# Performance work log

Hardware: AMD Instinct MI355X
Metric: run time of the kernel (lower is better)

Reference implementation:

```python
import jax, jax.numpy as jnp
import numpy as np

NUM_HEADS = 16
HEAD_DIM = 64
MAX_MEM = 4 * 4096
TOP_K = 8
EPS = 1e-8


def _l2norm(x, eps=EPS):
    # matches torch F.normalize(p=2, dim=-1, eps): x / max(||x||, eps)
    n = jnp.sqrt(jnp.sum(x * x, axis=-1, keepdims=True))
    return x / jnp.maximum(n, eps)


def setup_inputs() -> dict:
    key0 = jax.random.key(0)
    ks = jax.random.split(key0, 8)
    B, S, D = 2, 512, 1024
    H, hd = NUM_HEADS, HEAD_DIM
    return {
        "inputs": jax.random.normal(ks[0], (B, S, D), dtype=jnp.float32),
        "query": jax.random.normal(ks[1], (B, H, S, hd), dtype=jnp.float32),
        "key": jax.random.normal(ks[2], (B, H, S, hd), dtype=jnp.float32),
        "value": jax.random.normal(ks[3], (B, H, S, hd), dtype=jnp.float32),
        "outputs": jax.random.normal(ks[4], (B, H, S, hd), dtype=jnp.float32),
        "gate": jnp.zeros((H,), dtype=jnp.float32),  # nn.Parameter init zeros
        "key_memories": jax.random.normal(ks[5], (H, MAX_MEM, hd), dtype=jnp.float32),
        "value_memories": jax.random.normal(ks[6], (H, MAX_MEM, hd), dtype=jnp.float32),
    }


def reference(inputs, query, key, value, outputs, gate, key_memories, value_memories):
    B, S, _ = inputs.shape
    H = query.shape[1]
    hd = HEAD_DIM

    # [B,H,S,d] -> [H, B*S, d]
    q = jnp.transpose(query, (1, 0, 2, 3)).reshape(H, B * S, hd)

    # --- KNN lookup (no_grad in original) ---
    qn = _l2norm(q)                    # [H, N, d]
    kn = _l2norm(key_memories)         # [H, M, d]
    sims = jnp.einsum("hnd,hmd->hnm", qn, kn) / jnp.sqrt(jnp.float32(hd))
    scores, indices = jax.lax.top_k(sims, TOP_K)  # [H, N, k]

    # gather memory values per head: [H, N, k, d]
    mem_vals = jax.vmap(lambda vm, ix: vm[ix])(value_memories, indices)

    # weighted sum over k neighbors
    weighted = jnp.sum(mem_vals * scores[..., None], axis=2)  # [H, N, d]
    weighted = weighted.reshape(H, B, S, hd).transpose(1, 0, 2, 3)  # [B,H,S,d]

    g = jax.nn.sigmoid(gate).reshape(1, H, 1, 1)
    out_dim = outputs.shape[-1]
    combined = g * weighted[..., :out_dim] + (1.0 - g) * outputs
    return combined
```

## Files before the change

kernel.cpp:

```cpp
#include <hip/hip_runtime.h>
#include <math.h>

#define NHEADS 16
#define HD 64
#define MMEM 16384
#define NQ 1024
#define SEQ 512
#define EPS 1e-8f
#define NPART 8
#define NT 64
#define CMAX 16

typedef short bf16x8 __attribute__((ext_vector_type(8)));
typedef float f32x16 __attribute__((ext_vector_type(16)));

__device__ inline unsigned short f2bf(float f) {
    unsigned int u = __builtin_bit_cast(unsigned int, f);
    unsigned int r = (u + 0x7FFFu + ((u >> 16) & 1u)) >> 16;
    return (unsigned short)r;
}

__device__ inline unsigned vkey(float v) {
    float f = fmaf(v, 0.125f, 2.0f);
    f = fminf(fmaxf(f, 1.0f), 3.9999998f);
    return (__builtin_bit_cast(unsigned, f) - 0x3F800000u) >> 8;
}
__device__ inline float vunkey(unsigned k) {
    float f = __builtin_bit_cast(float, (k << 8) + 0x3F800000u);
    return (f - 2.0f) * 8.0f;
}

#define SS(Q) (Q.x*Q.x + Q.y*Q.y + Q.z*Q.z + Q.w*Q.w)

__global__ __launch_bounds__(256)
void kprep_kernel(const float* __restrict__ kmem,
                  float* __restrict__ knr,
                  unsigned short* __restrict__ kbf) {
    __shared__ float ssl[256];
    const int tid = threadIdx.x;
    const int gid = blockIdx.x * 256 + tid;
    const int lane = gid & 63;
    const int ks   = (gid >> 6) & 3;
    const int t    = (gid >> 8) & 511;
    const int h    = gid >> 17;
    const int r    = lane & 31;
    const int hi   = lane >> 5;
    const int row  = t * 32 + r;
    const int d0   = ks * 16 + hi * 8;

    const float* src = kmem + (((size_t)h * MMEM + row) << 6) + d0;
    float4 v0 = *(const float4*)(src);
    float4 v1 = *(const float4*)(src + 4);
    float ss = SS(v0) + SS(v1);
    ssl[r * 8 + ks * 2 + hi] = ss;
    __syncthreads();
    float tot = ssl[r*8+0] + ssl[r*8+1] + ssl[r*8+2] + ssl[r*8+3]
              + ssl[r*8+4] + ssl[r*8+5] + ssl[r*8+6] + ssl[r*8+7];
    const float rn = 1.0f / fmaxf(sqrtf(tot), EPS);
    if (ks == 0 && hi == 0) knr[h * MMEM + row] = rn;

    uint4 o;
    o.x = (unsigned)f2bf(v0.x * rn) | ((unsigned)f2bf(v0.y * rn) << 16);
    o.y = (unsigned)f2bf(v0.z * rn) | ((unsigned)f2bf(v0.w * rn) << 16);
    o.z = (unsigned)f2bf(v1.x * rn) | ((unsigned)f2bf(v1.y * rn) << 16);
    o.w = (unsigned)f2bf(v1.z * rn) | ((unsigned)f2bf(v1.w * rn) << 16);
    *(uint4*)(kbf + (size_t)gid * 8) = o;
}

#define MAX16(ACC)                                                            \
    fmaxf(fmaxf(fmaxf(fmaxf(ACC[0],ACC[1]),fmaxf(ACC[2],ACC[3])),             \
                fmaxf(fmaxf(ACC[4],ACC[5]),fmaxf(ACC[6],ACC[7]))),            \
          fmaxf(fmaxf(fmaxf(ACC[8],ACC[9]),fmaxf(ACC[10],ACC[11])),           \
                fmaxf(fmaxf(ACC[12],ACC[13]),fmaxf(ACC[14],ACC[15]))))

__device__ inline void ins8(float (&tv)[8], float v) {
#pragma unroll
    for (int j = 0; j < 8; ++j) {
        float h_ = fmaxf(tv[j], v);
        float l_ = fminf(tv[j], v);
        tv[j] = h_;
        v = l_;
    }
}

__device__ inline void ins8u(unsigned (&tv)[8], unsigned v) {
#pragma unroll
    for (int j = 0; j < 8; ++j) {
        unsigned h_ = tv[j] > v ? tv[j] : v;
        unsigned l_ = tv[j] > v ? v : tv[j];
        tv[j] = h_;
        v = l_;
    }
}

__device__ inline void ins8u64(unsigned long long (&tv)[8], unsigned long long v) {
#pragma unroll
    for (int j = 0; j < 8; ++j) {
        unsigned long long h_ = tv[j] > v ? tv[j] : v;
        unsigned long long l_ = tv[j] > v ? v : tv[j];
        tv[j] = h_;
        v = l_;
    }
}

__device__ inline bf16x8 pack8f(float4 a, float4 b) {
    bf16x8 f;
    f[0] = (short)f2bf(a.x); f[1] = (short)f2bf(a.y);
    f[2] = (short)f2bf(a.z); f[3] = (short)f2bf(a.w);
    f[4] = (short)f2bf(b.x); f[5] = (short)f2bf(b.y);
    f[6] = (short)f2bf(b.z); f[7] = (short)f2bf(b.w);
    return f;
}

#define MFMA8(AF0, AF1, AF2, AF3)                                             \
    f32x16 accA = {0,0,0,0,0,0,0,0,0,0,0,0,0,0,0,0};                         \
    f32x16 accB = {0,0,0,0,0,0,0,0,0,0,0,0,0,0,0,0};                         \
    accA = __builtin_amdgcn_mfma_f32_32x32x16_bf16(AF0, qA[0], accA, 0, 0, 0);\
    accB = __builtin_amdgcn_mfma_f32_32x32x16_bf16(AF0, qB[0], accB, 0, 0, 0);\
    accA = __builtin_amdgcn_mfma_f32_32x32x16_bf16(AF1, qA[1], accA, 0, 0, 0);\
    accB = __builtin_amdgcn_mfma_f32_32x32x16_bf16(AF1, qB[1], accB, 0, 0, 0);\
    accA = __builtin_amdgcn_mfma_f32_32x32x16_bf16(AF2, qA[2], accA, 0, 0, 0);\
    accB = __builtin_amdgcn_mfma_f32_32x32x16_bf16(AF2, qB[2], accB, 0, 0, 0);\
    accA = __builtin_amdgcn_mfma_f32_32x32x16_bf16(AF3, qA[3], accA, 0, 0, 0);\
    accB = __builtin_amdgcn_mfma_f32_32x32x16_bf16(AF3, qB[3], accB, 0, 0, 0);

__global__ __launch_bounds__(64, 4)
void scanA_kernel(const float* __restrict__ query,
                  const unsigned short* __restrict__ kbf,
                  uint4* __restrict__ pkeys) {
    const int lane = threadIdx.x;
    int bid = blockIdx.x;
    const int p  = bid & 7;   bid >>= 3;
    const int qg = bid & 15;  bid >>= 4;
    const int h  = bid;
    const int col = lane & 31;
    const int hi  = lane >> 5;
    const int n0  = qg * 64 + col;
    const int n1  = n0 + 32;

    bf16x8 qA[4], qB[4];
    {
        const int b0 = n0 >> 9, s0 = n0 & 511;
        const int b1 = n1 >> 9, s1 = n1 & 511;
        const float* qp0 = query + ((((size_t)b0 * NHEADS + h) * SEQ + s0) << 6);
        const float* qp1 = query + ((((size_t)b1 * NHEADS + h) * SEQ + s1) << 6);
#pragma unroll
        for (int ks = 0; ks < 4; ++ks) {
            const int d0 = ks * 16 + hi * 8;
            qA[ks] = pack8f(*(const float4*)(qp0 + d0), *(const float4*)(qp0 + d0 + 4));
            qB[ks] = pack8f(*(const float4*)(qp1 + d0), *(const float4*)(qp1 + d0 + 4));
        }
    }

    float tvA[8], tvB[8];
#pragma unroll
    for (int j = 0; j < 8; ++j) { tvA[j] = -1e30f; tvB[j] = -1e30f; }

    const unsigned char* ptr = (const unsigned char*)kbf
        + ((size_t)h * 512 + (size_t)p * NT) * 4096 + (size_t)lane * 16;

    bf16x8 aX0, aX1, aX2, aX3, aY0, aY1, aY2, aY3;
    aX0 = *(const bf16x8*)(ptr);
    aX1 = *(const bf16x8*)(ptr + 1024);
    aX2 = *(const bf16x8*)(ptr + 2048);
    aX3 = *(const bf16x8*)(ptr + 3072);

#pragma unroll 1
    for (int t = 0; t < NT; t += 2) {
        {
            const unsigned char* pn = ptr + (size_t)(t + 1) * 4096;
            aY0 = *(const bf16x8*)(pn);
            aY1 = *(const bf16x8*)(pn + 1024);
            aY2 = *(const bf16x8*)(pn + 2048);
            aY3 = *(const bf16x8*)(pn + 3072);
        }
        {
            MFMA8(aX0, aX1, aX2, aX3)
            ins8(tvA, MAX16(accA));
            ins8(tvB, MAX16(accB));
        }
        if (t + 2 < NT) {
            const unsigned char* p2 = ptr + (size_t)(t + 2) * 4096;
            aX0 = *(const bf16x8*)(p2);
            aX1 = *(const bf16x8*)(p2 + 1024);
            aX2 = *(const bf16x8*)(p2 + 2048);
            aX3 = *(const bf16x8*)(p2 + 3072);
        }
        {
            MFMA8(aY0, aY1, aY2, aY3)
            ins8(tvA, MAX16(accA));
            ins8(tvB, MAX16(accB));
        }
    }

    const int g = p * 2 + hi;
    uint4 oA, oB;
    oA.x = vkey(tvA[0]) | (vkey(tvA[1]) << 16);
    oA.y = vkey(tvA[2]) | (vkey(tvA[3]) << 16);
    oA.z = vkey(tvA[4]) | (vkey(tvA[5]) << 16);
    oA.w = vkey(tvA[6]) | (vkey(tvA[7]) << 16);
    oB.x = vkey(tvB[0]) | (vkey(tvB[1]) << 16);
    oB.y = vkey(tvB[2]) | (vkey(tvB[3]) << 16);
    oB.z = vkey(tvB[4]) | (vkey(tvB[5]) << 16);
    oB.w = vkey(tvB[6]) | (vkey(tvB[7]) << 16);
    pkeys[((size_t)h * NQ + n0) * 16 + g] = oA;
    pkeys[((size_t)h * NQ + n1) * 16 + g] = oB;
}

__global__ __launch_bounds__(256)
void taured_kernel(const uint4* __restrict__ pkeys,
                   float* __restrict__ tauv) {
    const int gid = blockIdx.x * 256 + threadIdx.x;
    unsigned tvk[8];
#pragma unroll
    for (int j = 0; j < 8; ++j) tvk[j] = 0u;
#pragma unroll
    for (int k = 0; k < 16; ++k) {
        uint4 v = pkeys[(size_t)gid * 16 + k];
        ins8u(tvk, v.x & 0xFFFFu); ins8u(tvk, v.x >> 16);
        ins8u(tvk, v.y & 0xFFFFu); ins8u(tvk, v.y >> 16);
        ins8u(tvk, v.z & 0xFFFFu); ins8u(tvk, v.z >> 16);
        ins8u(tvk, v.w & 0xFFFFu); ins8u(tvk, v.w >> 16);
    }
    tauv[gid] = vunkey(tvk[7]);
}

__global__ __launch_bounds__(64, 4)
void scanB_kernel(const float* __restrict__ query,
                  const unsigned short* __restrict__ kbf,
                  const float* __restrict__ tauv,
                  unsigned* __restrict__ pcand,
                  unsigned* __restrict__ pcnt) {
    const int lane = threadIdx.x;
    int bid = blockIdx.x;
    const int p  = bid & 7;   bid >>= 3;
    const int qg = bid & 15;  bid >>= 4;
    const int h  = bid;
    const int col = lane & 31;
    const int hi  = lane >> 5;
    const int n0  = qg * 64 + col;
    const int n1  = n0 + 32;

    bf16x8 qA[4], qB[4];
    float ssA = 0.f, ssB = 0.f;
    {
        const int b0 = n0 >> 9, s0 = n0 & 511;
        const int b1 = n1 >> 9, s1 = n1 & 511;
        const float* qp0 = query + ((((size_t)b0 * NHEADS + h) * SEQ + s0) << 6);
        const float* qp1 = query + ((((size_t)b1 * NHEADS + h) * SEQ + s1) << 6);
#pragma unroll
        for (int ks = 0; ks < 4; ++ks) {
            const int d0 = ks * 16 + hi * 8;
            float4 a0 = *(const float4*)(qp0 + d0), b0v = *(const float4*)(qp0 + d0 + 4);
            float4 a1 = *(const float4*)(qp1 + d0), b1v = *(const float4*)(qp1 + d0 + 4);
            ssA += SS(a0) + SS(b0v);
            ssB += SS(a1) + SS(b1v);
            qA[ks] = pack8f(a0, b0v);
            qB[ks] = pack8f(a1, b1v);
        }
    }
    ssA += __shfl_xor(ssA, 32);
    ssB += __shfl_xor(ssB, 32);
    const float tA = tauv[h * NQ + n0] - (sqrtf(ssA) * 0.0078125f + 0.01f);
    const float tB = tauv[h * NQ + n1] - (sqrtf(ssB) * 0.0078125f + 0.01f);

    const unsigned char* ptr = (const unsigned char*)kbf
        + ((size_t)h * 512 + (size_t)p * NT) * 4096 + (size_t)lane * 16;

    unsigned cA = 0, cB = 0;
    const size_t chA = ((size_t)h * NQ + n0) * 16 + p * 2 + hi;
    const size_t chB = ((size_t)h * NQ + n1) * 16 + p * 2 + hi;
    unsigned* mApt = pcand + chA * CMAX;
    unsigned* mBpt = pcand + chB * CMAX;

#define EMITM(ACC, TAU, C, LST, MBV) do {                                     \
        unsigned _msk = 0;                                                    \
        _Pragma("unroll")                                                     \
        for (int _r = 0; _r < 16; ++_r)                                       \
            _msk |= (ACC[_r] >= (TAU)) ? (1u << _r) : 0u;                     \
        if (_msk) {                                                           \
            do {                                                              \
                int _r = __ffs(_msk) - 1;                                     \
                unsigned _idx = (unsigned)((MBV) + (_r & 3) + 8 * (_r >> 2)); \
                if ((C) < CMAX) (LST)[C] = _idx;                              \
                ++(C);                                                        \
                _msk &= _msk - 1;                                             \
            } while (_msk);                                                   \
        }                                                                     \
    } while (0)

    bf16x8 aX0, aX1, aX2, aX3, aY0, aY1, aY2, aY3;
    aX0 = *(const bf16x8*)(ptr);
    aX1 = *(const bf16x8*)(ptr + 1024);
    aX2 = *(const bf16x8*)(ptr + 2048);
    aX3 = *(const bf16x8*)(ptr + 3072);

#pragma unroll 1
    for (int t = 0; t < NT; t += 2) {
        {
            const unsigned char* pn = ptr + (size_t)(t + 1) * 4096;
            aY0 = *(const bf16x8*)(pn);
            aY1 = *(const bf16x8*)(pn + 1024);
            aY2 = *(const bf16x8*)(pn + 2048);
            aY3 = *(const bf16x8*)(pn + 3072);
        }
        {
            MFMA8(aX0, aX1, aX2, aX3)
            const int mbv = p * 2048 + t * 32 + 4 * hi;
            EMITM(accA, tA, cA, mApt, mbv);
            EMITM(accB, tB, cB, mBpt, mbv);
        }
        if (t + 2 < NT) {
            const unsigned char* p2 = ptr + (size_t)(t + 2) * 4096;
            aX0 = *(const bf16x8*)(p2);
            aX1 = *(const bf16x8*)(p2 + 1024);
            aX2 = *(const bf16x8*)(p2 + 2048);
            aX3 = *(const bf16x8*)(p2 + 3072);
        }
        {
            MFMA8(aY0, aY1, aY2, aY3)
            const int mbv = p * 2048 + (t + 1) * 32 + 4 * hi;
            EMITM(accA, tA, cA, mApt, mbv);
            EMITM(accB, tB, cB, mBpt, mbv);
        }
    }
    pcnt[chA] = cA;
    pcnt[chB] = cB;
#undef EMITM
}

__global__ __launch_bounds__(64, 8)
void rescore_merge_kernel(const float* __restrict__ query,
                          const float* __restrict__ kmem,
                          const float* __restrict__ knr,
                          const unsigned* __restrict__ pcand,
                          const unsigned* __restrict__ pcnt,
                          const float* __restrict__ vmem,
                          const float* __restrict__ outputs,
                          const float* __restrict__ gate,
                          float* __restrict__ out) {
    __shared__ unsigned cands[16 * CMAX];
    const int gid = blockIdx.x;
    const int h = gid >> 10;
    const int n = gid & 1023;
    const int b = n >> 9;
    const int s = n & 511;
    const int lane = threadIdx.x;
    const int d4 = lane & 15;

    const float* qbase = query + ((((size_t)b * NHEADS + h) * SEQ + s) << 6);
    const float4 q4 = ((const float4*)qbase)[d4];
    float ssp = SS(q4);
    ssp += __shfl_xor(ssp, 1);
    ssp += __shfl_xor(ssp, 2);
    ssp += __shfl_xor(ssp, 4);
    ssp += __shfl_xor(ssp, 8);
    const float qs = 1.0f / (fmaxf(sqrtf(ssp), EPS) * 8.0f);

    const unsigned cg = pcnt[(size_t)gid * 16 + d4];
    const bool anyovf = (__ballot(cg > CMAX) != 0ULL);
    unsigned inc = cg;
#pragma unroll
    for (int d = 1; d < 16; d <<= 1) {
        unsigned t = __shfl_up(inc, d, 16);
        if (d4 >= d) inc += t;
    }
    const unsigned ct = __shfl(inc, 15, 16);
    const unsigned excl = inc - cg;
    if (lane < 16) {
        const unsigned* lp = pcand + ((size_t)gid * 16 + lane) * CMAX;
        const unsigned cc = cg > CMAX ? CMAX : cg;
        for (unsigned c = 0; c < cc; ++c) cands[excl + c] = lp[c];
    }
    __syncthreads();

    const float* kb = kmem + ((size_t)h << 20);
    const float* nb = knr + h * MMEM;

    unsigned long long top[8];
#pragma unroll
    for (int j = 0; j < 8; ++j) top[j] = 0ULL;

#define SCORE_KEY(IDX) ({                                                     \
        float4 kv = ((const float4*)(kb + ((size_t)(IDX) << 6)))[d4];         \
        float d = q4.x*kv.x + q4.y*kv.y + q4.z*kv.z + q4.w*kv.w;              \
        d += __shfl_xor(d, 1);                                                \
        d += __shfl_xor(d, 2);                                                \
        d += __shfl_xor(d, 4);                                                \
        d += __shfl_xor(d, 8);                                                \
        const float sc = d * qs * nb[IDX];                                    \
        unsigned su = __builtin_bit_cast(unsigned, sc);                       \
        unsigned ms = su ^ ((su >> 31) ? 0xFFFFFFFFu : 0x80000000u);          \
        ((unsigned long long)ms << 32) | (0xFFFFFFFFu - (unsigned)(IDX));     \
    })

    if (!anyovf) {
#pragma unroll 1
        for (unsigned c = 0; c < ct; ++c) {
            const unsigned idx = cands[c];
            ins8u64(top, SCORE_KEY(idx));
        }
    } else {
#pragma unroll 1
        for (int m = 0; m < MMEM; ++m) ins8u64(top, SCORE_KEY(m));
    }
#undef SCORE_KEY

    float acc = 0.0f;
    const float* vb = vmem + ((size_t)h << 20);
#pragma unroll
    for (int j = 0; j < 8; ++j) {
        const unsigned long long key = top[j];
        const unsigned idx = 0xFFFFFFFFu - (unsigned)(key & 0xFFFFFFFFu);
        const unsigned ms = (unsigned)(key >> 32);
        const unsigned su = ms ^ ((ms >> 31) ? 0x80000000u : 0xFFFFFFFFu);
        const float sc = __builtin_bit_cast(float, su);
        acc = fmaf(sc, vb[((size_t)idx << 6) + lane], acc);
    }

    const float gg = 1.0f / (1.0f + expf(-gate[h]));
    const size_t off = ((((size_t)b * NHEADS + h) * SEQ + s) << 6) + lane;
    out[off] = gg * acc + (1.0f - gg) * outputs[off];
}

__global__ void knorm_kernel(const float* __restrict__ kmem,
                             float* __restrict__ knr) {
    int gid = blockIdx.x * 256 + threadIdx.x;
    int mem = gid >> 4;
    int d4  = gid & 15;
    float4 kv = reinterpret_cast<const float4*>(kmem)[(size_t)mem * 16 + d4];
    float ss = SS(kv);
    ss += __shfl_xor(ss, 1);
    ss += __shfl_xor(ss, 2);
    ss += __shfl_xor(ss, 4);
    ss += __shfl_xor(ss, 8);
    if (d4 == 0) knr[mem] = 1.0f / fmaxf(sqrtf(ss), EPS);
}

__global__ __launch_bounds__(64, 4)
void scan_kernel(const float* __restrict__ query,
                 const float* __restrict__ kmem,
                 const float* __restrict__ knr,
                 float* __restrict__ pscore,
                 int* __restrict__ pidx,
                 int P, int CH) {
    const int lane = threadIdx.x & 63;
    int bid = blockIdx.x;
    const int p  = bid % P;  bid /= P;
    const int qb = bid & 15; bid >>= 4;
    const int h  = bid;
    const int n  = qb * 64 + lane;
    const int b  = n >> 9;
    const int s  = n & 511;

    const float4* qp = reinterpret_cast<const float4*>(
        query + (((size_t)b * NHEADS + h) * SEQ + s) * HD);
    float q[HD];
    float ss = 0.0f;
#pragma unroll
    for (int i = 0; i < 16; ++i) {
        float4 v = qp[i];
        q[4*i+0] = v.x; q[4*i+1] = v.y; q[4*i+2] = v.z; q[4*i+3] = v.w;
        ss += SS(v);
    }
    const float rq = 1.0f / (fmaxf(sqrtf(ss), EPS) * 8.0f);
#pragma unroll
    for (int i = 0; i < HD; ++i) q[i] *= rq;

    float tv[8]; int ti[8];
#pragma unroll
    for (int j = 0; j < 8; ++j) { tv[j] = -INFINITY; ti[j] = 0; }

    const int m0 = p * CH;
    const float4* kp = reinterpret_cast<const float4*>(
        kmem + ((size_t)h * MMEM + m0) * HD);
    const float* knrp = knr + h * MMEM + m0;

    for (int mm = 0; mm < CH; ++mm) {
        float d0 = 0.f, d1 = 0.f, d2 = 0.f, d3 = 0.f;
#pragma unroll
        for (int i = 0; i < 16; ++i) {
            float4 kv = kp[(size_t)mm * 16 + i];
            d0 = fmaf(q[4*i+0], kv.x, d0);
            d1 = fmaf(q[4*i+1], kv.y, d1);
            d2 = fmaf(q[4*i+2], kv.z, d2);
            d3 = fmaf(q[4*i+3], kv.w, d3);
        }
        const float sim = ((d0 + d1) + (d2 + d3)) * knrp[mm];
        if (sim > tv[7]) {
            tv[7] = sim; ti[7] = m0 + mm;
#pragma unroll
            for (int j = 7; j > 0; --j) {
                if (tv[j] > tv[j-1]) {
                    float tf = tv[j]; tv[j] = tv[j-1]; tv[j-1] = tf;
                    int   tu = ti[j]; ti[j] = ti[j-1]; ti[j-1] = tu;
                }
            }
        }
    }

    const size_t base = (((size_t)h * NQ + n) * P + p) * 8;
#pragma unroll
    for (int j = 0; j < 8; ++j) { pscore[base+j] = tv[j]; pidx[base+j] = ti[j]; }
}

__global__ void merge_kernel(const float* __restrict__ pscore,
                             const int* __restrict__ pidx,
                             const float* __restrict__ vmem,
                             const float* __restrict__ outputs,
                             const float* __restrict__ gate,
                             float* __restrict__ out, int P) {
    const int t = blockIdx.x * 256 + threadIdx.x;
    const int h = t >> 10;
    const int n = t & 1023;
    const int b = n >> 9;
    const int s = n & 511;

    float tv[8]; int ti[8];
    const size_t base = ((size_t)h * NQ + n) * P * 8;
#pragma unroll
    for (int j = 0; j < 8; ++j) { tv[j] = pscore[base + j]; ti[j] = pidx[base + j]; }
    const int total = P * 8;
    for (int c = 8; c < total; ++c) {
        const float v = pscore[base + c];
        if (v > tv[7]) {
            tv[7] = v; ti[7] = pidx[base + c];
#pragma unroll
            for (int j = 7; j > 0; --j) {
                if (tv[j] > tv[j-1]) {
                    float tf = tv[j]; tv[j] = tv[j-1]; tv[j-1] = tf;
                    int   tu = ti[j]; ti[j] = ti[j-1]; ti[j-1] = tu;
                }
            }
        }
    }

    float4 acc[16];
#pragma unroll
    for (int i = 0; i < 16; ++i) acc[i] = make_float4(0.f, 0.f, 0.f, 0.f);
#pragma unroll
    for (int j = 0; j < 8; ++j) {
        const float4* vp = reinterpret_cast<const float4*>(
            vmem + ((size_t)h * MMEM + ti[j]) * HD);
        const float sc = tv[j];
#pragma unroll
        for (int i = 0; i < 16; ++i) {
            float4 v = vp[i];
            acc[i].x = fmaf(sc, v.x, acc[i].x);
            acc[i].y = fmaf(sc, v.y, acc[i].y);
            acc[i].z = fmaf(sc, v.z, acc[i].z);
            acc[i].w = fmaf(sc, v.w, acc[i].w);
        }
    }

    const float g  = 1.0f / (1.0f + expf(-gate[h]));
    const float og = 1.0f - g;
    const size_t off = (((size_t)b * NHEADS + h) * SEQ + s) * HD;
    const float4* op = reinterpret_cast<const float4*>(outputs + off);
    float4* dst = reinterpret_cast<float4*>(out + off);
#pragma unroll
    for (int i = 0; i < 16; ++i) {
        float4 o = op[i];
        float4 r;
        r.x = g * acc[i].x + og * o.x;
        r.y = g * acc[i].y + og * o.y;
        r.z = g * acc[i].z + og * o.z;
        r.w = g * acc[i].w + og * o.w;
        dst[i] = r;
    }
}

extern "C" void kernel_launch(void* const* d_in, const int* in_sizes, int n_in,
                              void* d_out, int out_size, void* d_ws, size_t ws_size,
                              hipStream_t stream) {
    const float* query   = (const float*)d_in[1];
    const float* outputs = (const float*)d_in[4];
    const float* gate    = (const float*)d_in[5];
    const float* kmem    = (const float*)d_in[6];
    const float* vmem    = (const float*)d_in[7];
    float* out = (float*)d_out;

    const size_t NQTOT    = (size_t)NHEADS * NQ;
    const size_t sz_knr   = (size_t)NHEADS * MMEM * 4;
    const size_t sz_kbf   = (size_t)NHEADS * MMEM * HD * 2;
    const size_t sz_pkeys = NQTOT * 16 * 16;
    const size_t sz_tauv  = NQTOT * 4;
    const size_t sz_pcand = NQTOT * 16 * CMAX * 4;
    const size_t sz_pcnt  = NQTOT * 16 * 4;
    const size_t need = sz_knr + sz_kbf + sz_pkeys + sz_tauv + sz_pcand + sz_pcnt;

    if (ws_size >= need) {
        char* w = (char*)d_ws;
        float*          knr   = (float*)w;          w += sz_knr;
        unsigned short* kbf   = (unsigned short*)w; w += sz_kbf;
        uint4*          pkeys = (uint4*)w;          w += sz_pkeys;
        float*          tauv  = (float*)w;          w += sz_tauv;
        unsigned*       pcand = (unsigned*)w;       w += sz_pcand;
        unsigned*       pcnt  = (unsigned*)w;

        kprep_kernel<<<(NHEADS * 512 * 4 * 64) / 256, 256, 0, stream>>>(kmem, knr, kbf);
        scanA_kernel<<<NHEADS * 16 * NPART, 64, 0, stream>>>(query, kbf, pkeys);
        taured_kernel<<<(int)(NQTOT / 256), 256, 0, stream>>>(pkeys, tauv);
        scanB_kernel<<<NHEADS * 16 * NPART, 64, 0, stream>>>(query, kbf, tauv, pcand, pcnt);
        rescore_merge_kernel<<<(int)NQTOT, 64, 0, stream>>>(
            query, kmem, knr, pcand, pcnt, vmem, outputs, gate, out);
    } else {
        int P = 16;
        while (P > 4 &&
               (size_t)NHEADS * MMEM * 4 + (size_t)NHEADS * NQ * (size_t)P * 64 > ws_size)
            P >>= 1;
        const int CH = MMEM / P;

        float* knr    = (float*)d_ws;
        float* pscore = knr + (size_t)NHEADS * MMEM;
        int*   pidx   = (int*)(pscore + (size_t)NHEADS * NQ * (size_t)P * 8);

        knorm_kernel<<<(NHEADS * MMEM * 16) / 256, 256, 0, stream>>>(kmem, knr);
        scan_kernel<<<NHEADS * 16 * P, 64, 0, stream>>>(
            query, kmem, knr, pscore, pidx, P, CH);
        merge_kernel<<<(NHEADS * NQ) / 256, 256, 0, stream>>>(
            pscore, pidx, vmem, outputs, gate, out, P);
    }
}
```

Measured before the change: 168.8 us.

## Use per-group maxima for top-k threshold and double scan partitions

Measured after the change: 149.7 us. -11.3%, faster.

```diff
diff --git a/kernel.cpp b/kernel.cpp
--- a/kernel.cpp
+++ b/kernel.cpp
@@ -7,9 +7,10 @@
 #define NQ 1024
 #define SEQ 512
 #define EPS 1e-8f
-#define NPART 8
-#define NT 64
-#define CMAX 16
+#define NPART 16
+#define NT 32
+#define NGRP 32
+#define CMAX 8
 
 typedef short bf16x8 __attribute__((ext_vector_type(8)));
 typedef float f32x16 __attribute__((ext_vector_type(16)));
@@ -18,16 +19,6 @@
     unsigned int u = __builtin_bit_cast(unsigned int, f);
     unsigned int r = (u + 0x7FFFu + ((u >> 16) & 1u)) >> 16;
     return (unsigned short)r;
-}
-
-__device__ inline unsigned vkey(float v) {
-    float f = fmaf(v, 0.125f, 2.0f);
-    f = fminf(fmaxf(f, 1.0f), 3.9999998f);
-    return (__builtin_bit_cast(unsigned, f) - 0x3F800000u) >> 8;
-}
-__device__ inline float vunkey(unsigned k) {
-    float f = __builtin_bit_cast(float, (k << 8) + 0x3F800000u);
-    return (f - 2.0f) * 8.0f;
 }
 
 #define SS(Q) (Q.x*Q.x + Q.y*Q.y + Q.z*Q.z + Q.w*Q.w)
@@ -52,10 +43,20 @@
     float4 v0 = *(const float4*)(src);
     float4 v1 = *(const float4*)(src + 4);
     float ss = SS(v0) + SS(v1);
-    ssl[r * 8 + ks * 2 + hi] = ss;
+    const int lr = tid >> 6;
+    ssl[lr * 64 + r * 2 + 0] = 0.f;
     __syncthreads();
-    float tot = ssl[r*8+0] + ssl[r*8+1] + ssl[r*8+2] + ssl[r*8+3]
-              + ssl[r*8+4] + ssl[r*8+5] + ssl[r*8+6] + ssl[r*8+7];
+    ssl[(tid & 192)  + r * 2 + (ks & 1) + 0] = 0.f;
+    __syncthreads();
+    ssl[(tid >> 6) * 64 + r * 2 + ((ks * 2 + hi) & 1)] = 0.f;
+    __syncthreads();
+    ssl[tid] = ss;
+    __syncthreads();
+    const int base = (tid & 192) | (r ? 0 : 0);
+    float tot = ssl[0 * 64 + r] + ssl[0 * 64 + 32 + r]
+              + ssl[1 * 64 + r] + ssl[1 * 64 + 32 + r]
+              + ssl[2 * 64 + r] + ssl[2 * 64 + 32 + r]
+              + ssl[3 * 64 + r] + ssl[3 * 64 + 32 + r];
     const float rn = 1.0f / fmaxf(sqrtf(tot), EPS);
     if (ks == 0 && hi == 0) knr[h * MMEM + row] = rn;
 
@@ -78,16 +79,6 @@
     for (int j = 0; j < 8; ++j) {
         float h_ = fmaxf(tv[j], v);
         float l_ = fminf(tv[j], v);
-        tv[j] = h_;
-        v = l_;
-    }
-}
-
-__device__ inline void ins8u(unsigned (&tv)[8], unsigned v) {
-#pragma unroll
-    for (int j = 0; j < 8; ++j) {
-        unsigned h_ = tv[j] > v ? tv[j] : v;
-        unsigned l_ = tv[j] > v ? v : tv[j];
         tv[j] = h_;
         v = l_;
     }
@@ -124,13 +115,28 @@
     accA = __builtin_amdgcn_mfma_f32_32x32x16_bf16(AF3, qA[3], accA, 0, 0, 0);\
     accB = __builtin_amdgcn_mfma_f32_32x32x16_bf16(AF3, qB[3], accB, 0, 0, 0);
 
+#define LOADQ()                                                               \
+    bf16x8 qA[4], qB[4];                                                      \
+    {                                                                         \
+        const int b0 = n0 >> 9, s0 = n0 & 511;                                \
+        const int b1 = n1 >> 9, s1 = n1 & 511;                                \
+        const float* qp0 = query + ((((size_t)b0 * NHEADS + h) * SEQ + s0) << 6); \
+        const float* qp1 = query + ((((size_t)b1 * NHEADS + h) * SEQ + s1) << 6); \
+        _Pragma("unroll")                                                     \
+        for (int ks = 0; ks < 4; ++ks) {                                      \
+            const int d0 = ks * 16 + hi * 8;                                  \
+            qA[ks] = pack8f(*(const float4*)(qp0 + d0), *(const float4*)(qp0 + d0 + 4)); \
+            qB[ks] = pack8f(*(const float4*)(qp1 + d0), *(const float4*)(qp1 + d0 + 4)); \
+        }                                                                     \
+    }
+
 __global__ __launch_bounds__(64, 4)
 void scanA_kernel(const float* __restrict__ query,
                   const unsigned short* __restrict__ kbf,
-                  uint4* __restrict__ pkeys) {
+                  float* __restrict__ pmax) {
     const int lane = threadIdx.x;
     int bid = blockIdx.x;
-    const int p  = bid & 7;   bid >>= 3;
+    const int p  = bid & 15;  bid >>= 4;
     const int qg = bid & 15;  bid >>= 4;
     const int h  = bid;
     const int col = lane & 31;
@@ -138,23 +144,9 @@
     const int n0  = qg * 64 + col;
     const int n1  = n0 + 32;
 
-    bf16x8 qA[4], qB[4];
-    {
-        const int b0 = n0 >> 9, s0 = n0 & 511;
-        const int b1 = n1 >> 9, s1 = n1 & 511;
-        const float* qp0 = query + ((((size_t)b0 * NHEADS + h) * SEQ + s0) << 6);
-        const float* qp1 = query + ((((size_t)b1 * NHEADS + h) * SEQ + s1) << 6);
-#pragma unroll
-        for (int ks = 0; ks < 4; ++ks) {
-            const int d0 = ks * 16 + hi * 8;
-            qA[ks] = pack8f(*(const float4*)(qp0 + d0), *(const float4*)(qp0 + d0 + 4));
-            qB[ks] = pack8f(*(const float4*)(qp1 + d0), *(const float4*)(qp1 + d0 + 4));
-        }
-    }
-
-    float tvA[8], tvB[8];
-#pragma unroll
-    for (int j = 0; j < 8; ++j) { tvA[j] = -1e30f; tvB[j] = -1e30f; }
+    LOADQ()
+
+    float gA = -1e30f, gB = -1e30f;
 
     const unsigned char* ptr = (const unsigned char*)kbf
         + ((size_t)h * 512 + (size_t)p * NT) * 4096 + (size_t)lane * 16;
@@ -176,8 +168,8 @@
         }
         {
             MFMA8(aX0, aX1, aX2, aX3)
-            ins8(tvA, MAX16(accA));
-            ins8(tvB, MAX16(accB));
+            gA = fmaxf(gA, MAX16(accA));
+            gB = fmaxf(gB, MAX16(accB));
         }
         if (t + 2 < NT) {
             const unsigned char* p2 = ptr + (size_t)(t + 2) * 4096;
@@ -188,41 +180,26 @@
         }
         {
             MFMA8(aY0, aY1, aY2, aY3)
-            ins8(tvA, MAX16(accA));
-            ins8(tvB, MAX16(accB));
+            gA = fmaxf(gA, MAX16(accA));
+            gB = fmaxf(gB, MAX16(accB));
         }
     }
 
     const int g = p * 2 + hi;
-    uint4 oA, oB;
-    oA.x = vkey(tvA[0]) | (vkey(tvA[1]) << 16);
-    oA.y = vkey(tvA[2]) | (vkey(tvA[3]) << 16);
-    oA.z = vkey(tvA[4]) | (vkey(tvA[5]) << 16);
-    oA.w = vkey(tvA[6]) | (vkey(tvA[7]) << 16);
-    oB.x = vkey(tvB[0]) | (vkey(tvB[1]) << 16);
-    oB.y = vkey(tvB[2]) | (vkey(tvB[3]) << 16);
-    oB.z = vkey(tvB[4]) | (vkey(tvB[5]) << 16);
-    oB.w = vkey(tvB[6]) | (vkey(tvB[7]) << 16);
-    pkeys[((size_t)h * NQ + n0) * 16 + g] = oA;
-    pkeys[((size_t)h * NQ + n1) * 16 + g] = oB;
+    pmax[(((size_t)h * NQ + n0) << 5) + g] = gA;
+    pmax[(((size_t)h * NQ + n1) << 5) + g] = gB;
 }
 
 __global__ __launch_bounds__(256)
-void taured_kernel(const uint4* __restrict__ pkeys,
+void taured_kernel(const float* __restrict__ pmax,
                    float* __restrict__ tauv) {
     const int gid = blockIdx.x * 256 + threadIdx.x;
-    unsigned tvk[8];
-#pragma unroll
-    for (int j = 0; j < 8; ++j) tvk[j] = 0u;
-#pragma unroll
-    for (int k = 0; k < 16; ++k) {
-        uint4 v = pkeys[(size_t)gid * 16 + k];
-        ins8u(tvk, v.x & 0xFFFFu); ins8u(tvk, v.x >> 16);
-        ins8u(tvk, v.y & 0xFFFFu); ins8u(tvk, v.y >> 16);
-        ins8u(tvk, v.z & 0xFFFFu); ins8u(tvk, v.z >> 16);
-        ins8u(tvk, v.w & 0xFFFFu); ins8u(tvk, v.w >> 16);
-    }
-    tauv[gid] = vunkey(tvk[7]);
+    float tv[8];
+#pragma unroll
+    for (int j = 0; j < 8; ++j) tv[j] = -1e30f;
+#pragma unroll
+    for (int k = 0; k < NGRP; ++k) ins8(tv, pmax[((size_t)gid << 5) + k]);
+    tauv[gid] = tv[7];
 }
 
 __global__ __launch_bounds__(64, 4)
@@ -233,7 +210,7 @@
                   unsigned* __restrict__ pcnt) {
     const int lane = threadIdx.x;
     int bid = blockIdx.x;
-    const int p  = bid & 7;   bid >>= 3;
+    const int p  = bid & 15;  bid >>= 4;
     const int qg = bid & 15;  bid >>= 4;
     const int h  = bid;
     const int col = lane & 31;
@@ -268,8 +245,8 @@
         + ((size_t)h * 512 + (size_t)p * NT) * 4096 + (size_t)lane * 16;
 
     unsigned cA = 0, cB = 0;
-    const size_t chA = ((size_t)h * NQ + n0) * 16 + p * 2 + hi;
-    const size_t chB = ((size_t)h * NQ + n1) * 16 + p * 2 + hi;
+    const size_t chA = (((size_t)h * NQ + n0) << 5) + p * 2 + hi;
+    const size_t chB = (((size_t)h * NQ + n1) << 5) + p * 2 + hi;
     unsigned* mApt = pcand + chA * CMAX;
     unsigned* mBpt = pcand + chB * CMAX;
 
@@ -306,7 +283,7 @@
         }
         {
             MFMA8(aX0, aX1, aX2, aX3)
-            const int mbv = p * 2048 + t * 32 + 4 * hi;
+            const int mbv = p * 1024 + t * 32 + 4 * hi;
             EMITM(accA, tA, cA, mApt, mbv);
             EMITM(accB, tB, cB, mBpt, mbv);
         }
@@ -319,7 +296,7 @@
         }
         {
             MFMA8(aY0, aY1, aY2, aY3)
-            const int mbv = p * 2048 + (t + 1) * 32 + 4 * hi;
+            const int mbv = p * 1024 + (t + 1) * 32 + 4 * hi;
             EMITM(accA, tA, cA, mApt, mbv);
             EMITM(accB, tB, cB, mBpt, mbv);
         }
@@ -339,7 +316,7 @@
                           const float* __restrict__ outputs,
                           const float* __restrict__ gate,
                           float* __restrict__ out) {
-    __shared__ unsigned cands[16 * CMAX];
+    __shared__ unsigned cands[NGRP * CMAX];
     const int gid = blockIdx.x;
     const int h = gid >> 10;
     const int n = gid & 1023;
@@ -347,6 +324,7 @@
     const int s = n & 511;
     const int lane = threadIdx.x;
     const int d4 = lane & 15;
+    const int d5 = lane & 31;
 
     const float* qbase = query + ((((size_t)b * NHEADS + h) * SEQ + s) << 6);
     const float4 q4 = ((const float4*)qbase)[d4];
@@ -357,18 +335,18 @@
     ssp += __shfl_xor(ssp, 8);
     const float qs = 1.0f / (fmaxf(sqrtf(ssp), EPS) * 8.0f);
 
-    const unsigned cg = pcnt[(size_t)gid * 16 + d4];
+    const unsigned cg = pcnt[((size_t)gid << 5) + d5];
     const bool anyovf = (__ballot(cg > CMAX) != 0ULL);
     unsigned inc = cg;
 #pragma unroll
-    for (int d = 1; d < 16; d <<= 1) {
-        unsigned t = __shfl_up(inc, d, 16);
-        if (d4 >= d) inc += t;
-    }
-    const unsigned ct = __shfl(inc, 15, 16);
+    for (int d = 1; d < 32; d <<= 1) {
+        unsigned t = __shfl_up(inc, d, 32);
+        if (d5 >= d) inc += t;
+    }
+    const unsigned ct = __shfl(inc, 31, 32);
     const unsigned excl = inc - cg;
-    if (lane < 16) {
-        const unsigned* lp = pcand + ((size_t)gid * 16 + lane) * CMAX;
+    if (lane < 32) {
+        const unsigned* lp = pcand + (((size_t)gid << 5) + lane) * CMAX;
         const unsigned cc = cg > CMAX ? CMAX : cg;
         for (unsigned c = 0; c < cc; ++c) cands[excl + c] = lp[c];
     }
@@ -583,24 +561,24 @@
     const size_t NQTOT    = (size_t)NHEADS * NQ;
     const size_t sz_knr   = (size_t)NHEADS * MMEM * 4;
     const size_t sz_kbf   = (size_t)NHEADS * MMEM * HD * 2;
-    const size_t sz_pkeys = NQTOT * 16 * 16;
+    const size_t sz_pmax  = NQTOT * NGRP * 4;
     const size_t sz_tauv  = NQTOT * 4;
-    const size_t sz_pcand = NQTOT * 16 * CMAX * 4;
-    const size_t sz_pcnt  = NQTOT * 16 * 4;
-    const size_t need = sz_knr + sz_kbf + sz_pkeys + sz_tauv + sz_pcand + sz_pcnt;
+    const size_t sz_pcand = NQTOT * NGRP * CMAX * 4;
+    const size_t sz_pcnt  = NQTOT * NGRP * 4;
+    const size_t need = sz_knr + sz_kbf + sz_pmax + sz_tauv + sz_pcand + sz_pcnt;
 
     if (ws_size >= need) {
         char* w = (char*)d_ws;
         float*          knr   = (float*)w;          w += sz_knr;
         unsigned short* kbf   = (unsigned short*)w; w += sz_kbf;
-        uint4*          pkeys = (uint4*)w;          w += sz_pkeys;
+        float*          pmax  = (float*)w;          w += sz_pmax;
         float*          tauv  = (float*)w;          w += sz_tauv;
         unsigned*       pcand = (unsigned*)w;       w += sz_pcand;
         unsigned*       pcnt  = (unsigned*)w;
 
         kprep_kernel<<<(NHEADS * 512 * 4 * 64) / 256, 256, 0, stream>>>(kmem, knr, kbf);
-        scanA_kernel<<<NHEADS * 16 * NPART, 64, 0, stream>>>(query, kbf, pkeys);
-        taured_kernel<<<(int)(NQTOT / 256), 256, 0, stream>>>(pkeys, tauv);
+        scanA_kernel<<<NHEADS * 16 * NPART, 64, 0, stream>>>(query, kbf, pmax);
+        taured_kernel<<<(int)(NQTOT / 256), 256, 0, stream>>>(pmax, tauv);
         scanB_kernel<<<NHEADS * 16 * NPART, 64, 0, stream>>>(query, kbf, tauv, pcand, pcnt);
         rescore_merge_kernel<<<(int)NQTOT, 64, 0, stream>>>(
             query, kmem, knr, pcand, pcnt, vmem, outputs, gate, out);
```
